# Kernel tuning notes

Hardware: AMD Instinct MI355X
Metric: run time of the kernel (lower is better)

The kernel has to match this reference:

```python
import jax, jax.numpy as jnp
import numpy as np

N_NODES = 50000
N_EDGES = 800000
D = 64        # node feature dim (and edge feature dim, and msg output dim)
H_MSG = 256   # msg MLP hidden
H_UPD = 256   # upd MLP hidden


def setup_inputs() -> dict:
    key = jax.random.key(0)
    ks = jax.random.split(key, 12)
    h = jax.random.normal(ks[0], (N_NODES, D), dtype=jnp.float32)
    e = jax.random.normal(ks[1], (N_EDGES, D), dtype=jnp.float32)
    senders = jax.random.randint(ks[2], (N_EDGES,), 0, N_NODES, dtype=jnp.int32)
    receivers = jax.random.randint(ks[3], (N_EDGES,), 0, N_NODES, dtype=jnp.int32)
    d_msg_in = D + 2 * D   # concat([e, hs, hr])
    d_upd_in = 2 * D       # concat([h, agg])
    sc = lambda fan_in: 1.0 / np.sqrt(fan_in)
    W_m1 = jax.random.normal(ks[4], (d_msg_in, H_MSG), dtype=jnp.float32) * sc(d_msg_in)
    b_m1 = jnp.zeros((H_MSG,), dtype=jnp.float32)
    W_m2 = jax.random.normal(ks[5], (H_MSG, D), dtype=jnp.float32) * sc(H_MSG)
    b_m2 = jnp.zeros((D,), dtype=jnp.float32)
    W_u1 = jax.random.normal(ks[6], (d_upd_in, H_UPD), dtype=jnp.float32) * sc(d_upd_in)
    b_u1 = jnp.zeros((H_UPD,), dtype=jnp.float32)
    W_u2 = jax.random.normal(ks[7], (H_UPD, D), dtype=jnp.float32) * sc(H_UPD)
    b_u2 = jnp.zeros((D,), dtype=jnp.float32)
    return {
        "h": h, "e": e, "senders": senders, "receivers": receivers,
        "W_m1": W_m1, "b_m1": b_m1, "W_m2": W_m2, "b_m2": b_m2,
        "W_u1": W_u1, "b_u1": b_u1, "W_u2": W_u2, "b_u2": b_u2,
    }


def reference(h, e, senders, receivers, W_m1, b_m1, W_m2, b_m2, W_u1, b_u1, W_u2, b_u2):
    # message phase: gather endpoints, concat, 2-layer MLP
    hs = h[senders]                                   # [E, D]
    hr = h[receivers]                                 # [E, D]
    m_in = jnp.concatenate([e, hs, hr], axis=-1)      # [E, 3D]
    m = jax.nn.relu(m_in @ W_m1 + b_m1) @ W_m2 + b_m2 # [E, D]
    # aggregate messages at receivers
    agg = jax.ops.segment_sum(m, receivers, num_segments=h.shape[0])  # [N, D]
    # node update MLP + residual
    u_in = jnp.concatenate([h, agg], axis=-1)         # [N, 2D]
    dh = jax.nn.relu(u_in @ W_u1 + b_u1) @ W_u2 + b_u2
    return h + dh
```

## Files before the change

### kernel.cpp

```cpp
#include <hip/hip_runtime.h>
#include <hip/hip_bf16.h>
#include <hip/hip_fp16.h>
#include <cstdint>
#include <cstddef>

#define NNODES 50000
#define NEDGES 800000
#define DF 64
#define KM 192
#define KU 128
#define SROW 264

typedef __bf16 bf16_t;
typedef __bf16 bf16x8 __attribute__((ext_vector_type(8)));
typedef __bf16 bf16x4 __attribute__((ext_vector_type(4)));
typedef float  f32x4  __attribute__((ext_vector_type(4)));
typedef _Float16 f16x2 __attribute__((ext_vector_type(2)));

__global__ void prep_kernel(const float* __restrict__ Wm1, const float* __restrict__ Wm2,
                            const float* __restrict__ Wu1, const float* __restrict__ Wu2,
                            bf16_t* __restrict__ wp)
{
    int idx = blockIdx.x * 256 + threadIdx.x;
    const float* src; int N; int off; int local;
    if (idx < 49152)       { src = Wm1; N = 256; off = 0;     local = idx; }
    else if (idx < 65536)  { src = Wm2; N = 64;  off = 49152; local = idx - 49152; }
    else if (idx < 98304)  { src = Wu1; N = 256; off = 65536; local = idx - 65536; }
    else if (idx < 114688) { src = Wu2; N = 64;  off = 98304; local = idx - 98304; }
    else return;
    int j    = local & 7;
    int l    = (local >> 3) & 63;
    int frag = local >> 9;
    int nct  = N >> 4;
    int kblk = frag / nct;
    int ct   = frag - kblk * nct;
    int k = kblk * 32 + (l >> 4) * 8 + j;
    int n = ct * 16 + (l & 15);
    wp[off + local] = (bf16_t)src[(size_t)k * N + n];
}

__device__ __forceinline__ void st_bf16x4(bf16_t* p, float4 v) {
    bf16x4 bv;
    bv[0] = (bf16_t)v.x; bv[1] = (bf16_t)v.y; bv[2] = (bf16_t)v.z; bv[3] = (bf16_t)v.w;
    *reinterpret_cast<bf16x4*>(p) = bv;
}

template<bool H2>
__global__ __launch_bounds__(512, 4)
void msg_kernel(const float* __restrict__ h, const float* __restrict__ efeat,
                const int* __restrict__ snd, const int* __restrict__ rcv,
                const bf16_t* __restrict__ Wp1, const float* __restrict__ b1,
                const bf16_t* __restrict__ Wp2, const float* __restrict__ b2,
                void* __restrict__ aggv)
{
    __shared__ bf16_t s_buf[128 * SROW];
    __shared__ int s_snd[128];
    __shared__ int s_rcv[128];

    const int t  = threadIdx.x;
    const int e0 = blockIdx.x * 128;

    if (t < 128)      s_snd[t]       = snd[e0 + t];
    else if (t < 256) s_rcv[t - 128] = rcv[e0 + t - 128];

    #pragma unroll
    for (int it = 0; it < 4; ++it) {
        int i = t + it * 512; int row = i >> 4; int col = (i & 15) * 4;
        float4 v = *reinterpret_cast<const float4*>(efeat + (size_t)(e0 + row) * DF + col);
        st_bf16x4(&s_buf[row * SROW + col], v);
    }
    __syncthreads();

    #pragma unroll
    for (int it = 0; it < 4; ++it) {
        int i = t + it * 512; int row = i >> 4; int col = (i & 15) * 4;
        float4 v = *reinterpret_cast<const float4*>(h + (size_t)s_snd[row] * DF + col);
        st_bf16x4(&s_buf[row * SROW + DF + col], v);
    }
    #pragma unroll
    for (int it = 0; it < 4; ++it) {
        int i = t + it * 512; int row = i >> 4; int col = (i & 15) * 4;
        float4 v = *reinterpret_cast<const float4*>(h + (size_t)s_rcv[row] * DF + col);
        st_bf16x4(&s_buf[row * SROW + 2 * DF + col], v);
    }
    __syncthreads();

    const int w = t >> 6;
    const int l = t & 63;
    const int q = l >> 4;
    const int r = l & 15;

    f32x4 acc[2][8];
    #pragma unroll
    for (int g = 0; g < 2; ++g)
        #pragma unroll
        for (int am = 0; am < 8; ++am) acc[g][am] = (f32x4){0.f, 0.f, 0.f, 0.f};

    #pragma unroll
    for (int kb = 0; kb < 6; ++kb) {
        bf16x8 b0 = *reinterpret_cast<const bf16x8*>(Wp1 + ((size_t)(kb * 16 + w * 2 + 0) * 64 + l) * 8);
        bf16x8 b1f = *reinterpret_cast<const bf16x8*>(Wp1 + ((size_t)(kb * 16 + w * 2 + 1) * 64 + l) * 8);
        #pragma unroll
        for (int am = 0; am < 8; ++am) {
            bf16x8 a = *reinterpret_cast<const bf16x8*>(&s_buf[(am * 16 + r) * SROW + kb * 32 + q * 8]);
            acc[0][am] = __builtin_amdgcn_mfma_f32_16x16x32_bf16(a, b0,  acc[0][am], 0, 0, 0);
            acc[1][am] = __builtin_amdgcn_mfma_f32_16x16x32_bf16(a, b1f, acc[1][am], 0, 0, 0);
        }
    }
    __syncthreads();

    #pragma unroll
    for (int g = 0; g < 2; ++g) {
        const int col1 = (w * 2 + g) * 16 + r;
        const float bias1 = b1[col1];
        #pragma unroll
        for (int am = 0; am < 8; ++am)
            #pragma unroll
            for (int j = 0; j < 4; ++j)
                s_buf[(am * 16 + q * 4 + j) * SROW + col1] =
                    (bf16_t)fmaxf(acc[g][am][j] + bias1, 0.f);
    }
    __syncthreads();

    const int m2  = w >> 2;
    const int ct2 = w & 3;
    f32x4 acc2[4];
    #pragma unroll
    for (int am = 0; am < 4; ++am) acc2[am] = (f32x4){0.f, 0.f, 0.f, 0.f};

    #pragma unroll
    for (int kb = 0; kb < 8; ++kb) {
        bf16x8 b = *reinterpret_cast<const bf16x8*>(Wp2 + ((size_t)(kb * 4 + ct2) * 64 + l) * 8);
        #pragma unroll
        for (int am = 0; am < 4; ++am) {
            bf16x8 a = *reinterpret_cast<const bf16x8*>(&s_buf[(m2 * 64 + am * 16 + r) * SROW + kb * 32 + q * 8]);
            acc2[am] = __builtin_amdgcn_mfma_f32_16x16x32_bf16(a, b, acc2[am], 0, 0, 0);
        }
    }

    if constexpr (H2) {
        _Float16* aggh = (_Float16*)aggv;
        const int  cp  = ct2 * 16 + (r & ~1);
        const bool odd = (r & 1);
        const float blo = b2[cp], bhi = b2[cp + 1];
        #pragma unroll
        for (int am = 0; am < 4; ++am) {
            float v0 = acc2[am][0], v1 = acc2[am][1], v2 = acc2[am][2], v3 = acc2[am][3];
            float p0 = __shfl_xor(v0, 1), p1 = __shfl_xor(v1, 1);
            float p2 = __shfl_xor(v2, 1), p3 = __shfl_xor(v3, 1);
            float loA = odd ? p2 : v0, hiA = odd ? v2 : p0;
            float loB = odd ? p3 : v1, hiB = odd ? v3 : p1;
            int jbase = odd ? 2 : 0;
            int erowA = m2 * 64 + am * 16 + q * 4 + jbase;
            f16x2 hA = { (_Float16)(loA + blo), (_Float16)(hiA + bhi) };
            f16x2 hB = { (_Float16)(loB + blo), (_Float16)(hiB + bhi) };
            __builtin_amdgcn_global_atomic_fadd_v2f16(
                (f16x2*)(aggh + (size_t)s_rcv[erowA]     * DF + cp), hA);
            __builtin_amdgcn_global_atomic_fadd_v2f16(
                (f16x2*)(aggh + (size_t)s_rcv[erowA + 1] * DF + cp), hB);
        }
    } else {
        float* agg = (float*)aggv;
        const float bias2 = b2[ct2 * 16 + r];
        #pragma unroll
        for (int am = 0; am < 4; ++am)
            #pragma unroll
            for (int j = 0; j < 4; ++j) {
                int erow = m2 * 64 + am * 16 + q * 4 + j;
                atomicAdd(agg + (size_t)s_rcv[erow] * DF + ct2 * 16 + r, acc2[am][j] + bias2);
            }
    }
}

template<bool H2>
__global__ __launch_bounds__(256, 4)
void upd_kernel(const float* __restrict__ h, const void* __restrict__ aggv,
                const bf16_t* __restrict__ Wp1, const float* __restrict__ b1,
                const bf16_t* __restrict__ Wp2, const float* __restrict__ b2,
                float* __restrict__ out)
{
    __shared__ bf16_t s_buf[64 * SROW];

    const int t  = threadIdx.x;
    const int n0 = blockIdx.x * 64;

    if constexpr (H2) {
        const _Float16* aggh = (const _Float16*)aggv;
        #pragma unroll
        for (int it = 0; it < 4; ++it) {
            int i = t + it * 256; int nn = i >> 4; int col = (i & 15) * 4;
            int node = n0 + nn;
            float4 v = {0.f, 0.f, 0.f, 0.f};
            if (node < NNODES) v = *reinterpret_cast<const float4*>(h + (size_t)node * DF + col);
            st_bf16x4(&s_buf[nn * SROW + col], v);
        }
        #pragma unroll
        for (int it = 0; it < 4; ++it) {
            int i = t + it * 256; int nn = i >> 4; int col = (i & 15) * 4;
            int node = n0 + nn;
            float4 v = {0.f, 0.f, 0.f, 0.f};
            if (node < NNODES) {
                f16x2 h01 = *reinterpret_cast<const f16x2*>(aggh + (size_t)node * DF + col);
                f16x2 h23 = *reinterpret_cast<const f16x2*>(aggh + (size_t)node * DF + col + 2);
                v.x = (float)h01[0]; v.y = (float)h01[1];
                v.z = (float)h23[0]; v.w = (float)h23[1];
            }
            st_bf16x4(&s_buf[nn * SROW + DF + col], v);
        }
    } else {
        const float* agg = (const float*)aggv;
        #pragma unroll
        for (int it = 0; it < 8; ++it) {
            int i = t + it * 256; int nn = i >> 5; int col = (i & 31) * 4;
            int node = n0 + nn;
            float4 v = {0.f, 0.f, 0.f, 0.f};
            if (node < NNODES) {
                const float* srcp = (col < DF) ? (h + (size_t)node * DF + col)
                                               : (agg + (size_t)node * DF + (col - DF));
                v = *reinterpret_cast<const float4*>(srcp);
            }
            st_bf16x4(&s_buf[nn * SROW + col], v);
        }
    }
    __syncthreads();

    const int w = t >> 6;
    const int l = t & 63;
    const int q = l >> 4;
    const int r = l & 15;

    f32x4 acc[4][4];
    #pragma unroll
    for (int g = 0; g < 4; ++g)
        #pragma unroll
        for (int am = 0; am < 4; ++am) acc[g][am] = (f32x4){0.f, 0.f, 0.f, 0.f};

    #pragma unroll
    for (int kb = 0; kb < 4; ++kb) {
        bf16x8 a[4];
        #pragma unroll
        for (int am = 0; am < 4; ++am)
            a[am] = *reinterpret_cast<const bf16x8*>(&s_buf[(am * 16 + r) * SROW + kb * 32 + q * 8]);
        #pragma unroll
        for (int g = 0; g < 4; ++g) {
            int ct = w * 4 + g;
            bf16x8 b = *reinterpret_cast<const bf16x8*>(Wp1 + ((size_t)(kb * 16 + ct) * 64 + l) * 8);
            #pragma unroll
            for (int am = 0; am < 4; ++am)
                acc[g][am] = __builtin_amdgcn_mfma_f32_16x16x32_bf16(a[am], b, acc[g][am], 0, 0, 0);
        }
    }
    __syncthreads();

    #pragma unroll
    for (int g = 0; g < 4; ++g) {
        int col = (w * 4 + g) * 16 + r;
        float bias = b1[col];
        #pragma unroll
        for (int am = 0; am < 4; ++am)
            #pragma unroll
            for (int j = 0; j < 4; ++j)
                s_buf[(am * 16 + q * 4 + j) * SROW + col] =
                    (bf16_t)fmaxf(acc[g][am][j] + bias, 0.f);
    }
    __syncthreads();

    f32x4 acc2[4];
    #pragma unroll
    for (int am = 0; am < 4; ++am) acc2[am] = (f32x4){0.f, 0.f, 0.f, 0.f};

    #pragma unroll
    for (int kb = 0; kb < 8; ++kb) {
        bf16x8 a[4];
        #pragma unroll
        for (int am = 0; am < 4; ++am)
            a[am] = *reinterpret_cast<const bf16x8*>(&s_buf[(am * 16 + r) * SROW + kb * 32 + q * 8]);
        bf16x8 b = *reinterpret_cast<const bf16x8*>(Wp2 + ((size_t)(kb * 4 + w) * 64 + l) * 8);
        #pragma unroll
        for (int am = 0; am < 4; ++am)
            acc2[am] = __builtin_amdgcn_mfma_f32_16x16x32_bf16(a[am], b, acc2[am], 0, 0, 0);
    }

    float bias2 = b2[w * 16 + r];
    #pragma unroll
    for (int am = 0; am < 4; ++am)
        #pragma unroll
        for (int j = 0; j < 4; ++j) {
            int node = n0 + am * 16 + q * 4 + j;
            if (node < NNODES) {
                int col = w * 16 + r;
                out[(size_t)node * DF + col] =
                    h[(size_t)node * DF + col] + acc2[am][j] + bias2;
            }
        }
}

extern "C" void kernel_launch(void* const* d_in, const int* in_sizes, int n_in,
                              void* d_out, int out_size, void* d_ws, size_t ws_size,
                              hipStream_t stream)
{
    const float* h    = (const float*)d_in[0];
    const float* e    = (const float*)d_in[1];
    const int*   snd  = (const int*)d_in[2];
    const int*   rcv  = (const int*)d_in[3];
    const float* W_m1 = (const float*)d_in[4];
    const float* b_m1 = (const float*)d_in[5];
    const float* W_m2 = (const float*)d_in[6];
    const float* b_m2 = (const float*)d_in[7];
    const float* W_u1 = (const float*)d_in[8];
    const float* b_u1 = (const float*)d_in[9];
    const float* W_u2 = (const float*)d_in[10];
    const float* b_u2 = (const float*)d_in[11];
    float* out = (float*)d_out;

    const size_t aggh_bytes = (size_t)NNODES * DF * sizeof(_Float16);
    const size_t wp_bytes   = 114688 * sizeof(bf16_t);

    const bool useH2 = (ws_size >= aggh_bytes + wp_bytes);

    void*   aggv;
    bf16_t* wp;
    size_t  agg_clear;
    if (useH2) {
        aggv = d_ws;
        wp   = (bf16_t*)((char*)d_ws + aggh_bytes);
        agg_clear = aggh_bytes;
    } else {
        aggv = out;
        wp   = (bf16_t*)d_ws;
        agg_clear = (size_t)NNODES * DF * sizeof(float);
    }

    bf16_t* Wp_m1 = wp;
    bf16_t* Wp_m2 = wp + 49152;
    bf16_t* Wp_u1 = wp + 65536;
    bf16_t* Wp_u2 = wp + 98304;

    prep_kernel<<<448, 256, 0, stream>>>(W_m1, W_m2, W_u1, W_u2, wp);
    (void)hipMemsetAsync(aggv, 0, agg_clear, stream);

    if (useH2) {
        msg_kernel<true><<<NEDGES / 128, 512, 0, stream>>>(h, e, snd, rcv,
                                                           Wp_m1, b_m1, Wp_m2, b_m2, aggv);
        upd_kernel<true><<<(NNODES + 63) / 64, 256, 0, stream>>>(h, aggv,
                                                                 Wp_u1, b_u1, Wp_u2, b_u2, out);
    } else {
        msg_kernel<false><<<NEDGES / 128, 512, 0, stream>>>(h, e, snd, rcv,
                                                            Wp_m1, b_m1, Wp_m2, b_m2, aggv);
        upd_kernel<false><<<(NNODES + 63) / 64, 256, 0, stream>>>(h, aggv,
                                                                  Wp_u1, b_u1, Wp_u2, b_u2, out);
    }
}
```

Measured before the change: 234.6 us.

## Make message kernel persistent with register-prefetched gathers for the next tile

The message kernel becomes a persistent grid of 512 blocks with 256 threads that stride over edge tiles. While computing the current tile, it prefetches the next tile's sender/receiver features and edge features into registers, plus indices two tiles ahead. The goal is to hide gather latency behind MFMA work. Each wave now owns 4 column groups, which raises register pressure, and barriers are replaced with a custom waitcnt+s_barrier.

After: 704.0 us. 3x slower.

```diff
diff --git a/kernel.cpp b/kernel.cpp
--- a/kernel.cpp
+++ b/kernel.cpp
@@ -7,15 +7,19 @@
 #define NNODES 50000
 #define NEDGES 800000
 #define DF 64
-#define KM 192
-#define KU 128
 #define SROW 264
+#define NT 6250
+#define GST 512
 
 typedef __bf16 bf16_t;
 typedef __bf16 bf16x8 __attribute__((ext_vector_type(8)));
 typedef __bf16 bf16x4 __attribute__((ext_vector_type(4)));
 typedef float  f32x4  __attribute__((ext_vector_type(4)));
 typedef _Float16 f16x2 __attribute__((ext_vector_type(2)));
+
+__device__ __forceinline__ void bar_lds() {
+    asm volatile("s_waitcnt lgkmcnt(0)\n\ts_barrier" ::: "memory");
+}
 
 __global__ void prep_kernel(const float* __restrict__ Wm1, const float* __restrict__ Wm2,
                             const float* __restrict__ Wu1, const float* __restrict__ Wu2,
@@ -46,7 +50,7 @@
 }
 
 template<bool H2>
-__global__ __launch_bounds__(512, 4)
+__global__ __launch_bounds__(256, 2)
 void msg_kernel(const float* __restrict__ h, const float* __restrict__ efeat,
                 const int* __restrict__ snd, const int* __restrict__ rcv,
                 const bf16_t* __restrict__ Wp1, const float* __restrict__ b1,
@@ -54,121 +58,192 @@
                 void* __restrict__ aggv)
 {
     __shared__ bf16_t s_buf[128 * SROW];
-    __shared__ int s_snd[128];
-    __shared__ int s_rcv[128];
-
-    const int t  = threadIdx.x;
-    const int e0 = blockIdx.x * 128;
-
-    if (t < 128)      s_snd[t]       = snd[e0 + t];
-    else if (t < 256) s_rcv[t - 128] = rcv[e0 + t - 128];
-
-    #pragma unroll
-    for (int it = 0; it < 4; ++it) {
-        int i = t + it * 512; int row = i >> 4; int col = (i & 15) * 4;
-        float4 v = *reinterpret_cast<const float4*>(efeat + (size_t)(e0 + row) * DF + col);
-        st_bf16x4(&s_buf[row * SROW + col], v);
-    }
-    __syncthreads();
-
-    #pragma unroll
-    for (int it = 0; it < 4; ++it) {
-        int i = t + it * 512; int row = i >> 4; int col = (i & 15) * 4;
-        float4 v = *reinterpret_cast<const float4*>(h + (size_t)s_snd[row] * DF + col);
-        st_bf16x4(&s_buf[row * SROW + DF + col], v);
-    }
-    #pragma unroll
-    for (int it = 0; it < 4; ++it) {
-        int i = t + it * 512; int row = i >> 4; int col = (i & 15) * 4;
-        float4 v = *reinterpret_cast<const float4*>(h + (size_t)s_rcv[row] * DF + col);
-        st_bf16x4(&s_buf[row * SROW + 2 * DF + col], v);
-    }
-    __syncthreads();
-
+    __shared__ int s_idx[2][2][128];
+
+    const int t = threadIdx.x;
     const int w = t >> 6;
     const int l = t & 63;
     const int q = l >> 4;
     const int r = l & 15;
 
-    f32x4 acc[2][8];
-    #pragma unroll
-    for (int g = 0; g < 2; ++g)
-        #pragma unroll
-        for (int am = 0; am < 8; ++am) acc[g][am] = (f32x4){0.f, 0.f, 0.f, 0.f};
-
-    #pragma unroll
-    for (int kb = 0; kb < 6; ++kb) {
-        bf16x8 b0 = *reinterpret_cast<const bf16x8*>(Wp1 + ((size_t)(kb * 16 + w * 2 + 0) * 64 + l) * 8);
-        bf16x8 b1f = *reinterpret_cast<const bf16x8*>(Wp1 + ((size_t)(kb * 16 + w * 2 + 1) * 64 + l) * 8);
-        #pragma unroll
-        for (int am = 0; am < 8; ++am) {
-            bf16x8 a = *reinterpret_cast<const bf16x8*>(&s_buf[(am * 16 + r) * SROW + kb * 32 + q * 8]);
-            acc[0][am] = __builtin_amdgcn_mfma_f32_16x16x32_bf16(a, b0,  acc[0][am], 0, 0, 0);
-            acc[1][am] = __builtin_amdgcn_mfma_f32_16x16x32_bf16(a, b1f, acc[1][am], 0, 0, 0);
-        }
-    }
-    __syncthreads();
-
-    #pragma unroll
-    for (int g = 0; g < 2; ++g) {
-        const int col1 = (w * 2 + g) * 16 + r;
-        const float bias1 = b1[col1];
-        #pragma unroll
-        for (int am = 0; am < 8; ++am)
-            #pragma unroll
-            for (int j = 0; j < 4; ++j)
-                s_buf[(am * 16 + q * 4 + j) * SROW + col1] =
-                    (bf16_t)fmaxf(acc[g][am][j] + bias1, 0.f);
-    }
-    __syncthreads();
-
-    const int m2  = w >> 2;
-    const int ct2 = w & 3;
-    f32x4 acc2[4];
-    #pragma unroll
-    for (int am = 0; am < 4; ++am) acc2[am] = (f32x4){0.f, 0.f, 0.f, 0.f};
-
-    #pragma unroll
-    for (int kb = 0; kb < 8; ++kb) {
-        bf16x8 b = *reinterpret_cast<const bf16x8*>(Wp2 + ((size_t)(kb * 4 + ct2) * 64 + l) * 8);
-        #pragma unroll
-        for (int am = 0; am < 4; ++am) {
-            bf16x8 a = *reinterpret_cast<const bf16x8*>(&s_buf[(m2 * 64 + am * 16 + r) * SROW + kb * 32 + q * 8]);
-            acc2[am] = __builtin_amdgcn_mfma_f32_16x16x32_bf16(a, b, acc2[am], 0, 0, 0);
-        }
-    }
-
-    if constexpr (H2) {
-        _Float16* aggh = (_Float16*)aggv;
-        const int  cp  = ct2 * 16 + (r & ~1);
-        const bool odd = (r & 1);
-        const float blo = b2[cp], bhi = b2[cp + 1];
-        #pragma unroll
-        for (int am = 0; am < 4; ++am) {
-            float v0 = acc2[am][0], v1 = acc2[am][1], v2 = acc2[am][2], v3 = acc2[am][3];
-            float p0 = __shfl_xor(v0, 1), p1 = __shfl_xor(v1, 1);
-            float p2 = __shfl_xor(v2, 1), p3 = __shfl_xor(v3, 1);
-            float loA = odd ? p2 : v0, hiA = odd ? v2 : p0;
-            float loB = odd ? p3 : v1, hiB = odd ? v3 : p1;
-            int jbase = odd ? 2 : 0;
-            int erowA = m2 * 64 + am * 16 + q * 4 + jbase;
-            f16x2 hA = { (_Float16)(loA + blo), (_Float16)(hiA + bhi) };
-            f16x2 hB = { (_Float16)(loB + blo), (_Float16)(hiB + bhi) };
-            __builtin_amdgcn_global_atomic_fadd_v2f16(
-                (f16x2*)(aggh + (size_t)s_rcv[erowA]     * DF + cp), hA);
-            __builtin_amdgcn_global_atomic_fadd_v2f16(
-                (f16x2*)(aggh + (size_t)s_rcv[erowA + 1] * DF + cp), hB);
-        }
-    } else {
-        float* agg = (float*)aggv;
-        const float bias2 = b2[ct2 * 16 + r];
-        #pragma unroll
-        for (int am = 0; am < 4; ++am)
-            #pragma unroll
-            for (int j = 0; j < 4; ++j) {
-                int erow = m2 * 64 + am * 16 + q * 4 + j;
-                atomicAdd(agg + (size_t)s_rcv[erow] * DF + ct2 * 16 + r, acc2[am][j] + bias2);
-            }
+    int tile = blockIdx.x;
+
+    float bias1v[4];
+    #pragma unroll
+    for (int g = 0; g < 4; ++g) bias1v[g] = b1[(w * 4 + g) * 16 + r];
+    const int  cp  = w * 16 + (r & ~1);
+    const bool odd = (r & 1);
+    const float blo = b2[cp], bhi = b2[cp + 1];
+    const float bias2s = b2[w * 16 + r];
+
+    if (t < 128) {
+        s_idx[0][0][t] = snd[(size_t)tile * 128 + t];
+        s_idx[0][1][t] = rcv[(size_t)tile * 128 + t];
+        if (tile + GST < NT) {
+            s_idx[1][0][t] = snd[(size_t)(tile + GST) * 128 + t];
+            s_idx[1][1][t] = rcv[(size_t)(tile + GST) * 128 + t];
+        }
+    }
+    bar_lds();
+    {
+        const size_t e0 = (size_t)tile * 128;
+        #pragma unroll
+        for (int it = 0; it < 8; ++it) {
+            int i = t + it * 256; int row = i >> 4; int c4 = (i & 15) * 4;
+            float4 v = *reinterpret_cast<const float4*>(efeat + (e0 + row) * DF + c4);
+            st_bf16x4(&s_buf[row * SROW + c4], v);
+        }
+        #pragma unroll
+        for (int it = 0; it < 8; ++it) {
+            int i = t + it * 256; int row = i >> 4; int c4 = (i & 15) * 4;
+            float4 v = *reinterpret_cast<const float4*>(h + (size_t)s_idx[0][0][row] * DF + c4);
+            st_bf16x4(&s_buf[row * SROW + DF + c4], v);
+        }
+        #pragma unroll
+        for (int it = 0; it < 8; ++it) {
+            int i = t + it * 256; int row = i >> 4; int c4 = (i & 15) * 4;
+            float4 v = *reinterpret_cast<const float4*>(h + (size_t)s_idx[0][1][row] * DF + c4);
+            st_bf16x4(&s_buf[row * SROW + 2 * DF + c4], v);
+        }
+    }
+    bar_lds();
+
+    for (int k = 0; tile < NT; tile += GST, ++k) {
+        const bool hn  = (tile + GST < NT);
+        const bool hn2 = (tile + 2 * GST < NT);
+        const int  pc  = k & 1;
+        const int  pn  = pc ^ 1;
+
+        float4 hs[8], hr[8];
+        if (hn) {
+            #pragma unroll
+            for (int it = 0; it < 8; ++it) {
+                int i = t + it * 256; int row = i >> 4; int c4 = (i & 15) * 4;
+                hs[it] = *reinterpret_cast<const float4*>(h + (size_t)s_idx[pn][0][row] * DF + c4);
+            }
+            #pragma unroll
+            for (int it = 0; it < 8; ++it) {
+                int i = t + it * 256; int row = i >> 4; int c4 = (i & 15) * 4;
+                hr[it] = *reinterpret_cast<const float4*>(h + (size_t)s_idx[pn][1][row] * DF + c4);
+            }
+        }
+        int nsnd = 0, nrcv = 0;
+        if (hn2 && t < 128) {
+            nsnd = snd[(size_t)(tile + 2 * GST) * 128 + t];
+            nrcv = rcv[(size_t)(tile + 2 * GST) * 128 + t];
+        }
+
+        f32x4 acc[4][8];
+        #pragma unroll
+        for (int g = 0; g < 4; ++g)
+            #pragma unroll
+            for (int am = 0; am < 8; ++am) acc[g][am] = (f32x4){0.f, 0.f, 0.f, 0.f};
+
+        #pragma unroll
+        for (int kb = 0; kb < 6; ++kb) {
+            bf16x8 bfr[4];
+            #pragma unroll
+            for (int g = 0; g < 4; ++g)
+                bfr[g] = *reinterpret_cast<const bf16x8*>(Wp1 + ((size_t)(kb * 16 + w * 4 + g) * 64 + l) * 8);
+            #pragma unroll
+            for (int am = 0; am < 8; ++am) {
+                bf16x8 a = *reinterpret_cast<const bf16x8*>(&s_buf[(am * 16 + r) * SROW + kb * 32 + q * 8]);
+                #pragma unroll
+                for (int g = 0; g < 4; ++g)
+                    acc[g][am] = __builtin_amdgcn_mfma_f32_16x16x32_bf16(a, bfr[g], acc[g][am], 0, 0, 0);
+            }
+        }
+        bar_lds();
+
+        #pragma unroll
+        for (int g = 0; g < 4; ++g) {
+            const int col1 = (w * 4 + g) * 16 + r;
+            #pragma unroll
+            for (int am = 0; am < 8; ++am)
+                #pragma unroll
+                for (int j = 0; j < 4; ++j)
+                    s_buf[(am * 16 + q * 4 + j) * SROW + col1] =
+                        (bf16_t)fmaxf(acc[g][am][j] + bias1v[g], 0.f);
+        }
+        bar_lds();
+
+        float4 ev[8];
+        if (hn) {
+            const size_t e0n = (size_t)(tile + GST) * 128;
+            #pragma unroll
+            for (int it = 0; it < 8; ++it) {
+                int i = t + it * 256; int row = i >> 4; int c4 = (i & 15) * 4;
+                ev[it] = *reinterpret_cast<const float4*>(efeat + (e0n + row) * DF + c4);
+            }
+        }
+
+        f32x4 acc2[8];
+        #pragma unroll
+        for (int am = 0; am < 8; ++am) acc2[am] = (f32x4){0.f, 0.f, 0.f, 0.f};
+
+        #pragma unroll
+        for (int kb = 0; kb < 8; ++kb) {
+            bf16x8 b = *reinterpret_cast<const bf16x8*>(Wp2 + ((size_t)(kb * 4 + w) * 64 + l) * 8);
+            #pragma unroll
+            for (int am = 0; am < 8; ++am) {
+                bf16x8 a = *reinterpret_cast<const bf16x8*>(&s_buf[(am * 16 + r) * SROW + kb * 32 + q * 8]);
+                acc2[am] = __builtin_amdgcn_mfma_f32_16x16x32_bf16(a, b, acc2[am], 0, 0, 0);
+            }
+        }
+
+        if constexpr (H2) {
+            _Float16* aggh = (_Float16*)aggv;
+            #pragma unroll
+            for (int am = 0; am < 8; ++am) {
+                float v0 = acc2[am][0], v1 = acc2[am][1], v2 = acc2[am][2], v3 = acc2[am][3];
+                float p0 = __shfl_xor(v0, 1), p1 = __shfl_xor(v1, 1);
+                float p2 = __shfl_xor(v2, 1), p3 = __shfl_xor(v3, 1);
+                float loA = odd ? p2 : v0, hiA = odd ? v2 : p0;
+                float loB = odd ? p3 : v1, hiB = odd ? v3 : p1;
+                int jbase = odd ? 2 : 0;
+                int erowA = am * 16 + q * 4 + jbase;
+                f16x2 hA = { (_Float16)(loA + blo), (_Float16)(hiA + bhi) };
+                f16x2 hB = { (_Float16)(loB + blo), (_Float16)(hiB + bhi) };
+                __builtin_amdgcn_global_atomic_fadd_v2f16(
+                    (f16x2*)(aggh + (size_t)s_idx[pc][1][erowA]     * DF + cp), hA);
+                __builtin_amdgcn_global_atomic_fadd_v2f16(
+                    (f16x2*)(aggh + (size_t)s_idx[pc][1][erowA + 1] * DF + cp), hB);
+            }
+        } else {
+            float* agg = (float*)aggv;
+            #pragma unroll
+            for (int am = 0; am < 8; ++am)
+                #pragma unroll
+                for (int j = 0; j < 4; ++j) {
+                    int erow = am * 16 + q * 4 + j;
+                    atomicAdd(agg + (size_t)s_idx[pc][1][erow] * DF + w * 16 + r,
+                              acc2[am][j] + bias2s);
+                }
+        }
+        bar_lds();
+
+        if (hn) {
+            #pragma unroll
+            for (int it = 0; it < 8; ++it) {
+                int i = t + it * 256; int row = i >> 4; int c4 = (i & 15) * 4;
+                st_bf16x4(&s_buf[row * SROW + c4], ev[it]);
+            }
+            #pragma unroll
+            for (int it = 0; it < 8; ++it) {
+                int i = t + it * 256; int row = i >> 4; int c4 = (i & 15) * 4;
+                st_bf16x4(&s_buf[row * SROW + DF + c4], hs[it]);
+            }
+            #pragma unroll
+            for (int it = 0; it < 8; ++it) {
+                int i = t + it * 256; int row = i >> 4; int c4 = (i & 15) * 4;
+                st_bf16x4(&s_buf[row * SROW + 2 * DF + c4], hr[it]);
+            }
+        }
+        if (hn2 && t < 128) {
+            s_idx[pc][0][t] = nsnd;
+            s_idx[pc][1][t] = nrcv;
+        }
+        bar_lds();
     }
 }
 
@@ -340,13 +415,13 @@
     (void)hipMemsetAsync(aggv, 0, agg_clear, stream);
 
     if (useH2) {
-        msg_kernel<true><<<NEDGES / 128, 512, 0, stream>>>(h, e, snd, rcv,
-                                                           Wp_m1, b_m1, Wp_m2, b_m2, aggv);
+        msg_kernel<true><<<GST, 256, 0, stream>>>(h, e, snd, rcv,
+                                                  Wp_m1, b_m1, Wp_m2, b_m2, aggv);
         upd_kernel<true><<<(NNODES + 63) / 64, 256, 0, stream>>>(h, aggv,
                                                                  Wp_u1, b_u1, Wp_u2, b_u2, out);
     } else {
-        msg_kernel<false><<<NEDGES / 128, 512, 0, stream>>>(h, e, snd, rcv,
-                                                            Wp_m1, b_m1, Wp_m2, b_m2, aggv);
+        msg_kernel<false><<<GST, 256, 0, stream>>>(h, e, snd, rcv,
+                                                   Wp_m1, b_m1, Wp_m2, b_m2, aggv);
         upd_kernel<false><<<(NNODES + 63) / 64, 256, 0, stream>>>(h, aggv,
                                                                   Wp_u1, b_u1, Wp_u2, b_u2, out);
     }
```
